# Optimization experiments

Measured on AMD Instinct MI355X. Metric: run time of the kernel, lower is better.

Reference implementation:

```python
import jax, jax.numpy as jnp
import numpy as np

L = 10


def setup_inputs() -> dict:
    key = jax.random.key(0)
    ks = jax.random.split(key, L + 1)
    N = 1_000_000
    inp = {"points": jax.random.normal(ks[0], (N, 3), dtype=jnp.float32)}
    inp["cob_1"] = jax.random.normal(ks[1], (3, 3), dtype=jnp.float32)
    for l in range(2, L + 1):
        # [2l+1, 3*(2l-1)] change-of-basis matrix for angular order l
        inp[f"cob_{l}"] = jax.random.normal(ks[l], (2 * l + 1, 3 * (2 * l - 1)), dtype=jnp.float32)
    return inp


def _harmonic_forward(points, cobs):
    # points: [..., 3]; cobs: list of L matrices (cob_1 .. cob_L)
    shape = points.shape[:-1]
    f0 = jnp.ones(shape + (1,), dtype=points.dtype)
    # order-1 feature: [..., 3]
    f1 = jnp.einsum('...i,ji->...j', points, cobs[0])
    feats = [f0, f1]
    prev = f1
    for l in range(2, L + 1):
        cob = cobs[l - 1]  # [2l+1, 3*(2l-1)]
        # outer product of previous order feature with order-1 feature, flattened
        f = jnp.einsum('...i,...j->...ij', prev, f1).reshape(shape + (-1,))  # [..., 3*(2l-1)]
        f = jnp.einsum('...i,ji->...j', f, cob)  # [..., 2l+1]
        feats.append(f)
        prev = f
    return jnp.concatenate(feats, axis=-1)  # [..., (L+1)^2]


def reference(points, cob_1, cob_2, cob_3, cob_4, cob_5, cob_6, cob_7, cob_8, cob_9, cob_10):
    cobs = [cob_1, cob_2, cob_3, cob_4, cob_5, cob_6, cob_7, cob_8, cob_9, cob_10]
    return _harmonic_forward(points, cobs)
```

## Files before the change

kernel.cpp:

```cpp
#include <hip/hip_runtime.h>

#define BS 256
#define NFEAT 121
#define SST 21


__device__ __forceinline__ float dot3(const float* __restrict__ c, float x, float y, float z) {
    return fmaf(c[2], z, fmaf(c[1], y, c[0] * x));
}

template<int LL, bool UPDATE_PREV>
__device__ __forceinline__ void step_l(const float* __restrict__ cob,
                                       float* srow, int colofs,
                                       float f1x, float f1y, float f1z,
                                       float* prev) {
    constexpr int IN  = 2 * LL - 1;
    constexpr int OUT = 2 * LL + 1;
    #pragma unroll 1
    for (int j = 0; j < OUT; ++j) {
        const float* __restrict__ crow = cob + j * (3 * IN);
        float acc = 0.f;
        #pragma unroll
        for (int a = 0; a < IN; ++a) {
            float s = dot3(crow + 3 * a, f1x, f1y, f1z);
            acc = fmaf(prev[a], s, acc);
        }
        srow[colofs + j] = acc;
    }
    if (UPDATE_PREV) {
        #pragma unroll
        for (int j = 0; j < OUT; ++j) prev[j] = srow[colofs + j];
    }
}

template<int W>
__device__ __forceinline__ void wave_flush(const float* slab,
                                           float* __restrict__ outw,
                                           int wrows, int lane) {
    constexpr int RPI   = 64 / W;
    constexpr int LANES = RPI * W;
    constexpr int ITERS = (64 + RPI - 1) / RPI;
    const int lr = lane / W;
    const int lc = lane - lr * W;
    if (lane < LANES) {
        const float* sp = slab + lr * SST + lc;
        float* __restrict__ gp = outw + lr * NFEAT + lc;
        if (wrows == 64) {
            #pragma unroll
            for (int k = 0; k < ITERS; ++k) {
                const bool safe = (k * RPI + RPI - 1) < 64;
                if (safe || (k * RPI + lr) < 64)
                    gp[k * RPI * NFEAT] = sp[k * RPI * SST];
            }
        } else {
            #pragma unroll
            for (int k = 0; k < ITERS; ++k) {
                if (k * RPI + lr < wrows)
                    gp[k * RPI * NFEAT] = sp[k * RPI * SST];
            }
        }
    }
}

__global__ __launch_bounds__(BS) void harmonic_kernel(
    const float* __restrict__ points,
    const float* __restrict__ cob1,  const float* __restrict__ cob2,
    const float* __restrict__ cob3,  const float* __restrict__ cob4,
    const float* __restrict__ cob5,  const float* __restrict__ cob6,
    const float* __restrict__ cob7,  const float* __restrict__ cob8,
    const float* __restrict__ cob9,  const float* __restrict__ cob10,
    float* __restrict__ out, int N) {
    __shared__ float sbuf[BS * SST];

    const int t    = threadIdx.x;
    const int lane = t & 63;
    const int w    = t >> 6;
    const long long p0    = (long long)blockIdx.x * BS;
    const long long wbase = p0 + (w << 6);
    const long long p     = wbase + lane;
    const bool active = p < (long long)N;

    long long nv = (long long)N - wbase;
    const int wrows = nv >= 64 ? 64 : (nv > 0 ? (int)nv : 0);

    float px = 0.f, py = 0.f, pz = 0.f;
    if (active) {
        px = points[p * 3 + 0];
        py = points[p * 3 + 1];
        pz = points[p * 3 + 2];
    }

    const float f1x = dot3(cob1 + 0, px, py, pz);
    const float f1y = dot3(cob1 + 3, px, py, pz);
    const float f1z = dot3(cob1 + 6, px, py, pz);

    float prev[21];
    prev[0] = f1x; prev[1] = f1y; prev[2] = f1z;

    float* srow       = sbuf + t * SST;
    const float* slab = sbuf + (w << 6) * SST;
    float* __restrict__ outw = out + wbase * NFEAT;

    srow[0] = 1.f;
    srow[1] = f1x; srow[2] = f1y; srow[3] = f1z;
    step_l<2, true>(cob2, srow, 4, f1x, f1y, f1z, prev);
    step_l<3, true>(cob3, srow, 9, f1x, f1y, f1z, prev);
    wave_flush<16>(slab, outw + 0, wrows, lane);

    step_l<4, true>(cob4, srow, 0, f1x, f1y, f1z, prev);
    step_l<5, true>(cob5, srow, 9, f1x, f1y, f1z, prev);
    wave_flush<20>(slab, outw + 16, wrows, lane);

    step_l<6, true>(cob6, srow, 0, f1x, f1y, f1z, prev);
    wave_flush<13>(slab, outw + 36, wrows, lane);

    step_l<7, true>(cob7, srow, 0, f1x, f1y, f1z, prev);
    wave_flush<15>(slab, outw + 49, wrows, lane);

    step_l<8, true>(cob8, srow, 0, f1x, f1y, f1z, prev);
    wave_flush<17>(slab, outw + 64, wrows, lane);

    step_l<9, true>(cob9, srow, 0, f1x, f1y, f1z, prev);
    wave_flush<19>(slab, outw + 81, wrows, lane);

    step_l<10, false>(cob10, srow, 0, f1x, f1y, f1z, prev);
    wave_flush<21>(slab, outw + 100, wrows, lane);
}

extern "C" void kernel_launch(void* const* d_in, const int* in_sizes, int n_in,
                              void* d_out, int out_size, void* d_ws, size_t ws_size,
                              hipStream_t stream) {
    const float* points = (const float*)d_in[0];
    const float* cob[10];
    for (int i = 0; i < 10; ++i) cob[i] = (const float*)d_in[1 + i];
    float* out = (float*)d_out;
    const int N = in_sizes[0] / 3;

    const int grid = (N + BS - 1) / BS;
    harmonic_kernel<<<grid, BS, 0, stream>>>(
        points,
        cob[0], cob[1], cob[2], cob[3], cob[4],
        cob[5], cob[6], cob[7], cob[8], cob[9],
        out, N);
}
```

Measured before the change: 806.2 us.

## Batch shared-memory staging into four wider drains with row-per-iteration stores

Widens each thread's shared-memory staging row to 37 floats so several angular orders are accumulated before each flush, cutting the wave drains from seven to four. The drain now has one lane per column and loops over all 64 rows, so each store instruction writes one contiguous row segment instead of packing several rows into one wavefront. This lowers the number of flush phases and their loop overhead. In exchange it uses more LDS per block, which can reduce occupancy, and leaves lanes idle during drains (up to 43 of 64 for the 21-column drain) with 64 serial store iterations per drain.

Measured after the change: 801.5 us. About the same (-0.6%).

```diff
diff --git a/kernel.cpp b/kernel.cpp
--- a/kernel.cpp
+++ b/kernel.cpp
@@ -2,7 +2,7 @@
 
 #define BS 256
 #define NFEAT 121
-#define SST 21
+#define SMAX 37
 
 
 __device__ __forceinline__ float dot3(const float* __restrict__ c, float x, float y, float z) {
@@ -21,10 +21,8 @@
         const float* __restrict__ crow = cob + j * (3 * IN);
         float acc = 0.f;
         #pragma unroll
-        for (int a = 0; a < IN; ++a) {
-            float s = dot3(crow + 3 * a, f1x, f1y, f1z);
-            acc = fmaf(prev[a], s, acc);
-        }
+        for (int a = 0; a < IN; ++a)
+            acc = fmaf(prev[a], dot3(crow + 3 * a, f1x, f1y, f1z), acc);
         srow[colofs + j] = acc;
     }
     if (UPDATE_PREV) {
@@ -33,31 +31,20 @@
     }
 }
 
-template<int W>
-__device__ __forceinline__ void wave_flush(const float* slab,
-                                           float* __restrict__ outw,
+template<int W, int C0>
+__device__ __forceinline__ void wave_drain(const float* slab, float* __restrict__ outw,
                                            int wrows, int lane) {
-    constexpr int RPI   = 64 / W;
-    constexpr int LANES = RPI * W;
-    constexpr int ITERS = (64 + RPI - 1) / RPI;
-    const int lr = lane / W;
-    const int lc = lane - lr * W;
-    if (lane < LANES) {
-        const float* sp = slab + lr * SST + lc;
-        float* __restrict__ gp = outw + lr * NFEAT + lc;
+    if (lane < W) {
+        const float* sp = slab + lane;
+        float* __restrict__ gp = outw + C0 + lane;
         if (wrows == 64) {
-            #pragma unroll
-            for (int k = 0; k < ITERS; ++k) {
-                const bool safe = (k * RPI + RPI - 1) < 64;
-                if (safe || (k * RPI + lr) < 64)
-                    gp[k * RPI * NFEAT] = sp[k * RPI * SST];
-            }
+            #pragma unroll 16
+            for (int r = 0; r < 64; ++r)
+                gp[r * NFEAT] = sp[r * SMAX];
         } else {
-            #pragma unroll
-            for (int k = 0; k < ITERS; ++k) {
-                if (k * RPI + lr < wrows)
-                    gp[k * RPI * NFEAT] = sp[k * RPI * SST];
-            }
+            #pragma unroll 4
+            for (int r = 0; r < 64; ++r)
+                if (r < wrows) gp[r * NFEAT] = sp[r * SMAX];
         }
     }
 }
@@ -70,16 +57,14 @@
     const float* __restrict__ cob7,  const float* __restrict__ cob8,
     const float* __restrict__ cob9,  const float* __restrict__ cob10,
     float* __restrict__ out, int N) {
-    __shared__ float sbuf[BS * SST];
+    __shared__ float sbuf[(BS / 64) * 64 * SMAX];
 
     const int t    = threadIdx.x;
     const int lane = t & 63;
     const int w    = t >> 6;
-    const long long p0    = (long long)blockIdx.x * BS;
-    const long long wbase = p0 + (w << 6);
+    const long long wbase = (long long)blockIdx.x * BS + ((long long)w << 6);
     const long long p     = wbase + lane;
     const bool active = p < (long long)N;
-
     long long nv = (long long)N - wbase;
     const int wrows = nv >= 64 ? 64 : (nv > 0 ? (int)nv : 0);
 
@@ -97,34 +82,28 @@
     float prev[21];
     prev[0] = f1x; prev[1] = f1y; prev[2] = f1z;
 
-    float* srow       = sbuf + t * SST;
-    const float* slab = sbuf + (w << 6) * SST;
+    float* slab = sbuf + w * (64 * SMAX);
+    float* srow = slab + lane * SMAX;
     float* __restrict__ outw = out + wbase * NFEAT;
 
     srow[0] = 1.f;
     srow[1] = f1x; srow[2] = f1y; srow[3] = f1z;
-    step_l<2, true>(cob2, srow, 4, f1x, f1y, f1z, prev);
-    step_l<3, true>(cob3, srow, 9, f1x, f1y, f1z, prev);
-    wave_flush<16>(slab, outw + 0, wrows, lane);
+    step_l<2, true>(cob2, srow, 4,  f1x, f1y, f1z, prev);
+    step_l<3, true>(cob3, srow, 9,  f1x, f1y, f1z, prev);
+    step_l<4, true>(cob4, srow, 16, f1x, f1y, f1z, prev);
+    step_l<5, true>(cob5, srow, 25, f1x, f1y, f1z, prev);
+    wave_drain<36, 0>(slab, outw, wrows, lane);
 
-    step_l<4, true>(cob4, srow, 0, f1x, f1y, f1z, prev);
-    step_l<5, true>(cob5, srow, 9, f1x, f1y, f1z, prev);
-    wave_flush<20>(slab, outw + 16, wrows, lane);
+    step_l<6, true>(cob6, srow, 0,  f1x, f1y, f1z, prev);
+    step_l<7, true>(cob7, srow, 13, f1x, f1y, f1z, prev);
+    wave_drain<28, 36>(slab, outw, wrows, lane);
 
-    step_l<6, true>(cob6, srow, 0, f1x, f1y, f1z, prev);
-    wave_flush<13>(slab, outw + 36, wrows, lane);
-
-    step_l<7, true>(cob7, srow, 0, f1x, f1y, f1z, prev);
-    wave_flush<15>(slab, outw + 49, wrows, lane);
-
-    step_l<8, true>(cob8, srow, 0, f1x, f1y, f1z, prev);
-    wave_flush<17>(slab, outw + 64, wrows, lane);
-
-    step_l<9, true>(cob9, srow, 0, f1x, f1y, f1z, prev);
-    wave_flush<19>(slab, outw + 81, wrows, lane);
+    step_l<8, true>(cob8, srow, 0,  f1x, f1y, f1z, prev);
+    step_l<9, true>(cob9, srow, 17, f1x, f1y, f1z, prev);
+    wave_drain<36, 64>(slab, outw, wrows, lane);
 
     step_l<10, false>(cob10, srow, 0, f1x, f1y, f1z, prev);
-    wave_flush<21>(slab, outw + 100, wrows, lane);
+    wave_drain<21, 100>(slab, outw, wrows, lane);
 }
 
 extern "C" void kernel_launch(void* const* d_in, const int* in_sizes, int n_in,
```
